# Kernel tuning notes

Hardware: AMD Instinct MI355X
Metric: run time of the kernel (lower is better)

## Reference

```python
import jax, jax.numpy as jnp
import numpy as np

B, H, OUT = 16384, 1024, 128
W_SCALE = 0.03  # ~1/sqrt(H) so attention logits / softmax stay well-conditioned


def setup_inputs() -> dict:
    key = jax.random.key(0)
    ks = jax.random.split(key, 12)
    return {
        "f1": jax.random.normal(ks[0], (B, H), jnp.float32),
        "f2": jax.random.normal(ks[1], (B, H), jnp.float32),
        "f3": jax.random.normal(ks[2], (B, H), jnp.float32),
        "f4": jax.random.normal(ks[3], (B, H), jnp.float32),
        "Wq": jax.random.normal(ks[4], (H, H), jnp.float32) * W_SCALE,
        "bq": jax.random.normal(ks[5], (H,), jnp.float32) * W_SCALE,
        "Wk": jax.random.normal(ks[6], (H, H), jnp.float32) * W_SCALE,
        "bk": jax.random.normal(ks[7], (H,), jnp.float32) * W_SCALE,
        "Wv": jax.random.normal(ks[8], (H, H), jnp.float32) * W_SCALE,
        "bv": jax.random.normal(ks[9], (H,), jnp.float32) * W_SCALE,
        "Wfc": jax.random.normal(ks[10], (H, OUT), jnp.float32) * W_SCALE,
        "bfc": jax.random.normal(ks[11], (OUT,), jnp.float32) * W_SCALE,
    }


def reference(f1, f2, f3, f4, Wq, bq, Wk, bk, Wv, bv, Wfc, bfc):
    # Stack the 4 backbone features: z [B, 4, H]
    z = jnp.stack([f1, f2, f3, f4], axis=1)
    q = z @ Wq + bq            # [B, 4, H]
    k = z @ Wk + bk            # [B, 4, H]
    v = z @ Wv + bv            # [B, 4, H]
    # Tiny 4x4 self-attention over the 4 model-feature tokens
    score = jax.nn.softmax(jnp.einsum('bth,bsh->bts', q, k), axis=-1)  # [B,4,4]
    att = jnp.einsum('bts,bsh->bth', score, v)                          # [B,4,H]
    x = jnp.sum(att, axis=1)                                            # [B,H]
    out = jax.nn.softmax(x @ Wfc + bfc, axis=-1)                        # [B,OUT]
    return (x, out)
```

## Files before the change

### kernel.cpp

```cpp
#include <hip/hip_runtime.h>
#include <hip/hip_bf16.h>
#include <stdint.h>

#define B_SZ 16384
#define H_SZ 1024
#define OUT_SZ 128

typedef __attribute__((ext_vector_type(4))) float f32x4;
typedef __attribute__((ext_vector_type(8))) _Float16 h16x8;
typedef unsigned short u16;
typedef unsigned int u32;

__device__ __forceinline__ u16 f2h(float f) {
  union { _Float16 h; u16 u; } v; v.h = (_Float16)f; return v.u;
}
__device__ __forceinline__ float h2f(u16 u) {
  union { u16 u; _Float16 h; } v; v.u = u; return (float)v.h;
}
__device__ __forceinline__ u32 pk2(float a, float b) {
  return (u32)f2h(a) | ((u32)f2h(b) << 16);
}

__device__ __forceinline__ void gl_lds16(const void* g, void* l) {
  __builtin_amdgcn_global_load_lds(
      (const __attribute__((address_space(1))) u32*)g,
      (__attribute__((address_space(3))) u32*)l, 16, 0, 0);
}

template<int MODE>
__global__ __launch_bounds__(512, 2) void gemm_nt256(
    const u16* __restrict__ Aptr, const u16* __restrict__ Bptr,
    int K,
    float* __restrict__ ep_f, u16* __restrict__ ep_b,
    const float* __restrict__ ep_v,
    const float* zf0, const float* zf1, const float* zf2, const float* zf3)
{
  constexpr int BM = 256, BN = 256, BK = 64;
  __shared__ __align__(16) u16 sA[2][BM * BK];
  __shared__ __align__(16) u16 sB[2][BN * BK];
  const int tid  = threadIdx.x;
  const int wave = tid >> 6;
  const int lane = tid & 63;
  const int qd   = lane >> 4;
  const int c16  = lane & 15;
  const int bm0  = blockIdx.x * BM;
  const int bn0  = blockIdx.y * BN;
  const int wm   = (wave >> 2) * 128;
  const int wn   = (wave & 3) * 64;
  const size_t FBS = (size_t)B_SZ * H_SZ;

  auto stage = [&](int buf, int k0) {
#pragma unroll
    for (int i = 0; i < 4; ++i) {
      int slot = tid + i * 512;
      int r = slot >> 3, c = slot & 7;
      int cc = c ^ (r & 7);
      {
        int gm = bm0 + r;
        const u16* gp;
        if (MODE == 1)
          gp = Aptr + (size_t)(gm & 3) * FBS + (size_t)(gm >> 2) * H_SZ + (k0 + cc * 8);
        else
          gp = Aptr + (size_t)gm * K + (k0 + cc * 8);
        gl_lds16(gp, &sA[buf][(size_t)(slot & ~63) * 8]);
      }
      {
        int gn = bn0 + r;
        const u16* gp = Bptr + (size_t)gn * K + (k0 + cc * 8);
        gl_lds16(gp, &sB[buf][(size_t)(slot & ~63) * 8]);
      }
    }
  };

  f32x4 acc[8][4];
#pragma unroll
  for (int i = 0; i < 8; ++i)
#pragma unroll
    for (int j = 0; j < 4; ++j)
      acc[i][j] = (f32x4){0.f, 0.f, 0.f, 0.f};

  stage(0, 0);
  __syncthreads();
  int cur = 0;
  for (int k0 = 0; k0 < K; k0 += BK) {
    if (k0 + BK < K) stage(cur ^ 1, k0 + BK);
#pragma unroll
    for (int ks = 0; ks < 2; ++ks) {
      h16x8 af[8], bfr[4];
#pragma unroll
      for (int im = 0; im < 8; ++im) {
        int m = wm + im * 16 + c16;
        af[im] = *(const h16x8*)&sA[cur][m * 64 + (((ks * 4 + qd) ^ (m & 7)) * 8)];
      }
#pragma unroll
      for (int in = 0; in < 4; ++in) {
        int n = wn + in * 16 + c16;
        bfr[in] = *(const h16x8*)&sB[cur][n * 64 + (((ks * 4 + qd) ^ (n & 7)) * 8)];
      }
#pragma unroll
      for (int im = 0; im < 8; ++im)
#pragma unroll
        for (int in = 0; in < 4; ++in)
          acc[im][in] = __builtin_amdgcn_mfma_f32_16x16x32_f16(af[im], bfr[in], acc[im][in], 0, 0, 0);
    }
    __syncthreads();
    cur ^= 1;
  }

  if constexpr (MODE == 1) {
    const float* zf[4] = {zf0, zf1, zf2, zf3};
    const int yg = (int)blockIdx.y * 4 + (wave & 3);
#pragma unroll
    for (int im = 0; im < 8; ++im) {
      int mrow = bm0 + wm + im * 16 + qd * 4;
      size_t b = (size_t)(mrow >> 2);
      float p[4][4];
#pragma unroll
      for (int r = 0; r < 4; ++r)
#pragma unroll
        for (int s = 0; s < 4; ++s) p[r][s] = 0.f;
#pragma unroll
      for (int in = 0; in < 4; ++in) {
        int n = bn0 + wn + in * 16 + c16;
        float akv = ep_v[n];
        float rv[4];
#pragma unroll
        for (int r = 0; r < 4; ++r) rv[r] = acc[im][in][r] + akv;
#pragma unroll
        for (int s = 0; s < 4; ++s) {
          float zv = zf[s][b * H_SZ + n];
#pragma unroll
          for (int r = 0; r < 4; ++r) p[r][s] += rv[r] * zv;
        }
      }
#pragma unroll
      for (int r = 0; r < 4; ++r)
#pragma unroll
        for (int s = 0; s < 4; ++s) {
          float v = p[r][s];
          v += __shfl_xor(v, 1);
          v += __shfl_xor(v, 2);
          v += __shfl_xor(v, 4);
          v += __shfl_xor(v, 8);
          if (c16 == 0) ep_f[(b * 16 + (size_t)(r * 4 + s)) * 16 + yg] = v;
        }
    }
  } else {
#pragma unroll
    for (int im = 0; im < 8; ++im)
#pragma unroll
      for (int in = 0; in < 4; ++in) {
        int n = bn0 + wn + in * 16 + c16;
        float bvv = 4.0f * ep_v[n];
#pragma unroll
        for (int r = 0; r < 4; ++r) {
          int m = bm0 + wm + im * 16 + qd * 4 + r;
          float v = acc[im][in][r] + bvv;
          ep_f[(size_t)m * H_SZ + n] = v;
          ep_b[(size_t)m * H_SZ + n] = f2h(v);
        }
      }
  }
}

template<int MODE>
__global__ __launch_bounds__(256, 4) void gemm_nt(
    const u16* __restrict__ Aptr, const u16* __restrict__ Bptr,
    int N, int K,
    float* __restrict__ ep_f, u16* __restrict__ ep_b,
    const float* __restrict__ ep_v)
{
  constexpr int BM = 128, BN = 128, BK = 32;
  __shared__ __align__(16) u16 sA[2][BM * BK];
  __shared__ __align__(16) u16 sB[2][BN * BK];
  const int tid  = threadIdx.x;
  const int wave = tid >> 6;
  const int lane = tid & 63;
  const int qd   = lane >> 4;
  const int c16  = lane & 15;
  const int bm0  = blockIdx.x * BM;
  const int bn0  = blockIdx.y * BN;
  const int wm   = (wave >> 1) * 64;
  const int wn   = (wave & 1) * 64;

  auto stage = [&](int buf, int k0) {
#pragma unroll
    for (int i = 0; i < 2; ++i) {
      int slot = tid + i * 256;
      int r = slot >> 2, pp = slot & 3;
      int cc = pp ^ ((r >> 1) & 3);
      {
        int gm = bm0 + r;
        const u16* gp = Aptr + (size_t)gm * K + (k0 + cc * 8);
        gl_lds16(gp, &sA[buf][(size_t)(slot & ~63) * 8]);
      }
      {
        int gn = bn0 + r;
        const u16* gp = Bptr + (size_t)gn * K + (k0 + cc * 8);
        gl_lds16(gp, &sB[buf][(size_t)(slot & ~63) * 8]);
      }
    }
  };

  f32x4 acc[4][4];
#pragma unroll
  for (int i = 0; i < 4; ++i)
#pragma unroll
    for (int j = 0; j < 4; ++j)
      acc[i][j] = (f32x4){0.f, 0.f, 0.f, 0.f};

  stage(0, 0);
  __syncthreads();
  int cur = 0;
  for (int k0 = 0; k0 < K; k0 += BK) {
    if (k0 + BK < K) stage(cur ^ 1, k0 + BK);
    h16x8 af[4], bfr[4];
#pragma unroll
    for (int im = 0; im < 4; ++im) {
      int m = wm + im * 16 + c16;
      int slot = m * 4 + (qd ^ ((m >> 1) & 3));
      af[im] = *(const h16x8*)&sA[cur][slot * 8];
    }
#pragma unroll
    for (int in = 0; in < 4; ++in) {
      int n = wn + in * 16 + c16;
      int slot = n * 4 + (qd ^ ((n >> 1) & 3));
      bfr[in] = *(const h16x8*)&sB[cur][slot * 8];
    }
#pragma unroll
    for (int im = 0; im < 4; ++im)
#pragma unroll
      for (int in = 0; in < 4; ++in)
        acc[im][in] = __builtin_amdgcn_mfma_f32_16x16x32_f16(af[im], bfr[in], acc[im][in], 0, 0, 0);
    __syncthreads();
    cur ^= 1;
  }

  if constexpr (MODE == 0) {
#pragma unroll
    for (int im = 0; im < 4; ++im)
#pragma unroll
      for (int in = 0; in < 4; ++in) {
        int n = bn0 + wn + in * 16 + c16;
#pragma unroll
        for (int r = 0; r < 4; ++r) {
          int m = bm0 + wm + im * 16 + qd * 4 + r;
          ep_b[(size_t)m * N + n] = f2h(acc[im][in][r]);
        }
      }
  } else {
#pragma unroll
    for (int im = 0; im < 4; ++im)
#pragma unroll
      for (int in = 0; in < 4; ++in) {
        int n = bn0 + wn + in * 16 + c16;
        float bc = ep_v[n];
#pragma unroll
        for (int r = 0; r < 4; ++r) {
          int m = bm0 + wm + im * 16 + qd * 4 + r;
          ep_f[(size_t)m * N + n] = acc[im][in][r] + bc;
        }
      }
  }
}

__global__ __launch_bounds__(256) void prep_weights(
    const float* __restrict__ Wq, const float* __restrict__ Wk,
    const float* __restrict__ Wv, const float* __restrict__ Wfc,
    const float* __restrict__ bq,
    u16* __restrict__ Wq16, u16* __restrict__ Wk16,
    u16* __restrict__ WvT, u16* __restrict__ WfcT,
    float* __restrict__ ak)
{
  __shared__ float t[32][33];
  int blk = blockIdx.x, tid = threadIdx.x;
  if (blk < 2048) {
    const float* src = (blk < 1024) ? Wq : Wk;
    u16* dst = (blk < 1024) ? Wq16 : Wk16;
    size_t i0 = (size_t)(blk & 1023) * 1024 + tid * 4;
    float4 v = *(const float4*)(src + i0);
    *(uint2*)(dst + i0) = make_uint2(pk2(v.x, v.y), pk2(v.z, v.w));
  } else if (blk < 3200) {
    int lx = tid & 31, ly = tid >> 5;
    if (blk < 3072) {
      int ti = blk - 2048;
      int tx = ti & 31, ty = ti >> 5;
#pragma unroll
      for (int k = 0; k < 4; ++k)
        t[ly + 8 * k][lx] = Wv[(size_t)(ty * 32 + ly + 8 * k) * 1024 + tx * 32 + lx];
      __syncthreads();
#pragma unroll
      for (int k = 0; k < 4; ++k)
        WvT[(size_t)(tx * 32 + ly + 8 * k) * 1024 + ty * 32 + lx] = f2h(t[lx][ly + 8 * k]);
    } else {
      int ti = blk - 3072;
      int tx = ti & 3, ty = ti >> 2;
#pragma unroll
      for (int k = 0; k < 4; ++k)
        t[ly + 8 * k][lx] = Wfc[(size_t)(ty * 32 + ly + 8 * k) * 128 + tx * 32 + lx];
      __syncthreads();
#pragma unroll
      for (int k = 0; k < 4; ++k)
        WfcT[(size_t)(tx * 32 + ly + 8 * k) * 1024 + ty * 32 + lx] = f2h(t[lx][ly + 8 * k]);
    }
  } else {
    int wave = tid >> 6, lane = tid & 63;
    int row = (blk - 3200) * 4 + wave;
    float s = 0.f;
    for (int i = lane; i < 1024; i += 64)
      s += Wk[(size_t)row * 1024 + i] * bq[i];
#pragma unroll
    for (int m = 1; m < 64; m <<= 1) s += __shfl_xor(s, m);
    if (lane == 0) ak[row] = s;
  }
}

__global__ __launch_bounds__(256) void convert4(
    const float* __restrict__ f1, const float* __restrict__ f2,
    const float* __restrict__ f3, const float* __restrict__ f4,
    u16* __restrict__ Zh)
{
  int a = blockIdx.x >> 13;
  const float* f = (a == 0) ? f1 : (a == 1) ? f2 : (a == 2) ? f3 : f4;
  size_t off = (size_t)(blockIdx.x & 8191) * 2048 + threadIdx.x * 8;
  float4 v0 = *(const float4*)(f + off);
  float4 v1 = *(const float4*)(f + off + 4);
  *(uint4*)(Zh + (size_t)a * B_SZ * H_SZ + off) =
      make_uint4(pk2(v0.x, v0.y), pk2(v0.z, v0.w), pk2(v1.x, v1.y), pk2(v1.z, v1.w));
}

__global__ __launch_bounds__(256) void softmax_g(
    const float* __restrict__ pl, const u16* __restrict__ Zh,
    u16* __restrict__ G)
{
  const size_t FBS = (size_t)B_SZ * H_SZ;
  int wave = threadIdx.x >> 6, lane = threadIdx.x & 63;
  size_t b = (size_t)blockIdx.x * 4 + wave;
  float4 pv = *(const float4*)(pl + b * 256 + (size_t)lane * 4);
  float part = pv.x + pv.y + pv.z + pv.w;
  part += __shfl_xor(part, 1);
  part += __shfl_xor(part, 2);
  float l[16];
#pragma unroll
  for (int i = 0; i < 16; ++i) l[i] = __shfl(part, i * 4);
  float w0 = 0, w1 = 0, w2 = 0, w3 = 0;
#pragma unroll
  for (int t = 0; t < 4; ++t) {
    float a0 = l[t * 4], a1 = l[t * 4 + 1], a2 = l[t * 4 + 2], a3 = l[t * 4 + 3];
    float mx = fmaxf(fmaxf(a0, a1), fmaxf(a2, a3));
    float e0 = __expf(a0 - mx), e1 = __expf(a1 - mx), e2 = __expf(a2 - mx), e3 = __expf(a3 - mx);
    float inv = 1.0f / (e0 + e1 + e2 + e3);
    w0 += e0 * inv; w1 += e1 * inv; w2 += e2 * inv; w3 += e3 * inv;
  }
#pragma unroll
  for (int ch = 0; ch < 2; ++ch) {
    size_t h0 = (size_t)lane * 8 + ch * 512;
    float g[8];
#pragma unroll
    for (int j = 0; j < 8; ++j) g[j] = 0.f;
#pragma unroll
    for (int s = 0; s < 4; ++s) {
      float ws = (s == 0) ? w0 : (s == 1) ? w1 : (s == 2) ? w2 : w3;
      uint4 zz = *(const uint4*)(Zh + (size_t)s * FBS + b * H_SZ + h0);
      u32 zs[4] = {zz.x, zz.y, zz.z, zz.w};
#pragma unroll
      for (int j = 0; j < 4; ++j) {
        g[2 * j]     += ws * h2f((u16)(zs[j] & 0xffffu));
        g[2 * j + 1] += ws * h2f((u16)(zs[j] >> 16));
      }
    }
    *(uint4*)(G + b * H_SZ + h0) =
        make_uint4(pk2(g[0], g[1]), pk2(g[2], g[3]), pk2(g[4], g[5]), pk2(g[6], g[7]));
  }
}

__global__ __launch_bounds__(256) void softmax_out(
    const float* __restrict__ L2, float* __restrict__ out)
{
  int wave = threadIdx.x >> 6, lane = threadIdx.x & 63;
  size_t row = (size_t)blockIdx.x * 4 + wave;
  float2 v = *(const float2*)(L2 + row * 128 + lane * 2);
  float mx = fmaxf(v.x, v.y);
#pragma unroll
  for (int m = 1; m < 64; m <<= 1) mx = fmaxf(mx, __shfl_xor(mx, m));
  float e0 = __expf(v.x - mx), e1 = __expf(v.y - mx);
  float s = e0 + e1;
#pragma unroll
  for (int m = 1; m < 64; m <<= 1) s += __shfl_xor(s, m);
  float inv = 1.0f / s;
  *(float2*)(out + row * 128 + lane * 2) = make_float2(e0 * inv, e1 * inv);
}

extern "C" void kernel_launch(void* const* d_in, const int* in_sizes, int n_in,
                              void* d_out, int out_size, void* d_ws, size_t ws_size,
                              hipStream_t stream)
{
  const float* f1  = (const float*)d_in[0];
  const float* f2  = (const float*)d_in[1];
  const float* f3  = (const float*)d_in[2];
  const float* f4  = (const float*)d_in[3];
  const float* Wq  = (const float*)d_in[4];
  const float* bq  = (const float*)d_in[5];
  const float* Wk  = (const float*)d_in[6];
  const float* Wv  = (const float*)d_in[8];
  const float* bv  = (const float*)d_in[9];
  const float* Wfc = (const float*)d_in[10];
  const float* bfc = (const float*)d_in[11];

  float* x_out = (float*)d_out;
  float* out2  = x_out + (size_t)B_SZ * H_SZ;

  const size_t BH = (size_t)B_SZ * H_SZ;
  const size_t HH = (size_t)H_SZ * H_SZ;
  char* w = (char*)d_ws;
  u16* Zh   = (u16*)w;  w += 4 * BH * sizeof(u16);
  u16* G    = (u16*)w;  w += BH * sizeof(u16);
  u16* Xh   = (u16*)w;  w += BH * sizeof(u16);
  u16* Wq16 = (u16*)w;  w += HH * 2;
  u16* Wk16 = (u16*)w;  w += HH * 2;
  u16* AT   = (u16*)w;  w += HH * 2;
  u16* WvT  = (u16*)w;  w += HH * 2;
  u16* WfcT = (u16*)w;  w += (size_t)OUT_SZ * H_SZ * 2;
  float* ak  = (float*)w;  w += H_SZ * sizeof(float);
  float* fcl = (float*)w;  w += (size_t)B_SZ * OUT_SZ * sizeof(float);
  float* pl  = (float*)Xh;

  prep_weights<<<3456, 256, 0, stream>>>(Wq, Wk, Wv, Wfc, bq,
      Wq16, Wk16, WvT, WfcT, ak);
  convert4<<<32768, 256, 0, stream>>>(f1, f2, f3, f4, Zh);
  gemm_nt<0><<<dim3(8, 8), 256, 0, stream>>>(
      Wk16, Wq16, 1024, 1024, nullptr, AT, nullptr);
  gemm_nt256<1><<<dim3(256, 4), 512, 0, stream>>>(
      Zh, AT, 1024, pl, nullptr, ak, f1, f2, f3, f4);
  softmax_g<<<4096, 256, 0, stream>>>(pl, Zh, G);
  gemm_nt256<2><<<dim3(64, 4), 512, 0, stream>>>(
      G, WvT, 1024, x_out, Xh, bv,
      nullptr, nullptr, nullptr, nullptr);
  gemm_nt<3><<<dim3(128, 1), 256, 0, stream>>>(
      Xh, WfcT, 128, 1024, fcl, nullptr, bfc);
  softmax_out<<<4096, 256, 0, stream>>>(fcl, out2);
}
```

Before: 686.0 us.

## Deepen GEMM pipeline to 4-stage LDS ring with vmcnt waits and fp16 epilogue reads

Reworks the main 256x256 GEMM loop so that BK drops to 32 and LDS uses a 4-buffer ring prefetched three tiles ahead. The full-block __syncthreads plus double buffer is replaced by s_waitcnt vmcnt with a single barrier per tile, and s_setprio is raised around the MFMA block. The swizzle is adapted to the narrower tile, and K is now a compile-time constant. The MODE 1 epilogue reads the fp16 Z copy instead of the fp32 features, which halves that traffic but adds fp16 rounding to the attention-score dot products.

```diff
diff --git a/kernel.cpp b/kernel.cpp
--- a/kernel.cpp
+++ b/kernel.cpp
@@ -30,14 +30,12 @@
 template<int MODE>
 __global__ __launch_bounds__(512, 2) void gemm_nt256(
     const u16* __restrict__ Aptr, const u16* __restrict__ Bptr,
-    int K,
     float* __restrict__ ep_f, u16* __restrict__ ep_b,
-    const float* __restrict__ ep_v,
-    const float* zf0, const float* zf1, const float* zf2, const float* zf3)
-{
-  constexpr int BM = 256, BN = 256, BK = 64;
-  __shared__ __align__(16) u16 sA[2][BM * BK];
-  __shared__ __align__(16) u16 sB[2][BN * BK];
+    const float* __restrict__ ep_v, const u16* __restrict__ Zep)
+{
+  constexpr int BM = 256, BN = 256, BK = 32, K = 1024, NT = K / BK;
+  __shared__ __align__(16) u16 sA[4][BM * BK];
+  __shared__ __align__(16) u16 sB[4][BN * BK];
   const int tid  = threadIdx.x;
   const int wave = tid >> 6;
   const int lane = tid & 63;
@@ -49,12 +47,13 @@
   const int wn   = (wave & 3) * 64;
   const size_t FBS = (size_t)B_SZ * H_SZ;
 
-  auto stage = [&](int buf, int k0) {
-#pragma unroll
-    for (int i = 0; i < 4; ++i) {
+  auto stage = [&](int buf, int t) {
+    const int k0 = t * BK;
+#pragma unroll
+    for (int i = 0; i < 2; ++i) {
       int slot = tid + i * 512;
-      int r = slot >> 3, c = slot & 7;
-      int cc = c ^ (r & 7);
+      int r = slot >> 2, c = slot & 3;
+      int cc = c ^ ((r >> 1) & 3);
       {
         int gm = bm0 + r;
         const u16* gp;
@@ -80,35 +79,41 @@
       acc[i][j] = (f32x4){0.f, 0.f, 0.f, 0.f};
 
   stage(0, 0);
-  __syncthreads();
-  int cur = 0;
-  for (int k0 = 0; k0 < K; k0 += BK) {
-    if (k0 + BK < K) stage(cur ^ 1, k0 + BK);
-#pragma unroll
-    for (int ks = 0; ks < 2; ++ks) {
-      h16x8 af[8], bfr[4];
-#pragma unroll
-      for (int im = 0; im < 8; ++im) {
-        int m = wm + im * 16 + c16;
-        af[im] = *(const h16x8*)&sA[cur][m * 64 + (((ks * 4 + qd) ^ (m & 7)) * 8)];
-      }
-#pragma unroll
-      for (int in = 0; in < 4; ++in) {
-        int n = wn + in * 16 + c16;
-        bfr[in] = *(const h16x8*)&sB[cur][n * 64 + (((ks * 4 + qd) ^ (n & 7)) * 8)];
-      }
-#pragma unroll
-      for (int im = 0; im < 8; ++im)
-#pragma unroll
-        for (int in = 0; in < 4; ++in)
-          acc[im][in] = __builtin_amdgcn_mfma_f32_16x16x32_f16(af[im], bfr[in], acc[im][in], 0, 0, 0);
-    }
-    __syncthreads();
-    cur ^= 1;
+  stage(1, 1);
+  stage(2, 2);
+
+  for (int t = 0; t < NT; ++t) {
+    const int buf = t & 3;
+    if (t + 2 < NT)      asm volatile("s_waitcnt vmcnt(8)" ::: "memory");
+    else if (t + 1 < NT) asm volatile("s_waitcnt vmcnt(4)" ::: "memory");
+    else                 asm volatile("s_waitcnt vmcnt(0)" ::: "memory");
+    __builtin_amdgcn_s_barrier();
+    asm volatile("" ::: "memory");
+    if (t + 3 < NT) stage((t + 3) & 3, t + 3);
+
+    h16x8 af[8], bfr[4];
+#pragma unroll
+    for (int im = 0; im < 8; ++im) {
+      int m = wm + im * 16 + c16;
+      int slot = m * 4 + (qd ^ ((m >> 1) & 3));
+      af[im] = *(const h16x8*)&sA[buf][slot * 8];
+    }
+#pragma unroll
+    for (int in = 0; in < 4; ++in) {
+      int n = wn + in * 16 + c16;
+      int slot = n * 4 + (qd ^ ((n >> 1) & 3));
+      bfr[in] = *(const h16x8*)&sB[buf][slot * 8];
+    }
+    __builtin_amdgcn_s_setprio(1);
+#pragma unroll
+    for (int im = 0; im < 8; ++im)
+#pragma unroll
+      for (int in = 0; in < 4; ++in)
+        acc[im][in] = __builtin_amdgcn_mfma_f32_16x16x32_f16(af[im], bfr[in], acc[im][in], 0, 0, 0);
+    __builtin_amdgcn_s_setprio(0);
   }
 
   if constexpr (MODE == 1) {
-    const float* zf[4] = {zf0, zf1, zf2, zf3};
     const int yg = (int)blockIdx.y * 4 + (wave & 3);
 #pragma unroll
     for (int im = 0; im < 8; ++im) {
@@ -128,7 +133,7 @@
         for (int r = 0; r < 4; ++r) rv[r] = acc[im][in][r] + akv;
 #pragma unroll
         for (int s = 0; s < 4; ++s) {
-          float zv = zf[s][b * H_SZ + n];
+          float zv = h2f(Zep[(size_t)s * FBS + b * H_SZ + n]);
 #pragma unroll
           for (int r = 0; r < 4; ++r) p[r][s] += rv[r] * zv;
         }
@@ -431,11 +436,10 @@
   gemm_nt<0><<<dim3(8, 8), 256, 0, stream>>>(
       Wk16, Wq16, 1024, 1024, nullptr, AT, nullptr);
   gemm_nt256<1><<<dim3(256, 4), 512, 0, stream>>>(
-      Zh, AT, 1024, pl, nullptr, ak, f1, f2, f3, f4);
+      Zh, AT, pl, nullptr, ak, Zh);
   softmax_g<<<4096, 256, 0, stream>>>(pl, Zh, G);
   gemm_nt256<2><<<dim3(64, 4), 512, 0, stream>>>(
-      G, WvT, 1024, x_out, Xh, bv,
-      nullptr, nullptr, nullptr, nullptr);
+      G, WvT, x_out, Xh, bv, nullptr);
   gemm_nt<3><<<dim3(128, 1), 256, 0, stream>>>(
       Xh, WfcT, 128, 1024, fcl, nullptr, bfc);
   softmax_out<<<4096, 256, 0, stream>>>(fcl, out2);
```

Result: no change. 678.9 us (-1.0%).

## Retile big GEMMs to 64x512 blocks and read fp16 Z in epilogue

Applied to the files above, without the earlier changes.

Replaces the 256x256x64 GEMM tile with a 64x512x32 tile in which all eight waves share the same 64 rows. The grid grows and launch bounds allow four blocks per SM, which lowers register pressure and raises occupancy. The MODE 1 epilogue now reads the fp16 converted Z buffer instead of the four fp32 feature arrays, halving those reads at some loss of precision. Smaller M tiles mean less reuse of the B operand, so each block reloads more weight data.

```diff
diff --git a/kernel.cpp b/kernel.cpp
--- a/kernel.cpp
+++ b/kernel.cpp
@@ -28,14 +28,12 @@
 }
 
 template<int MODE>
-__global__ __launch_bounds__(512, 2) void gemm_nt256(
+__global__ __launch_bounds__(512, 4) void gemm_nt64(
     const u16* __restrict__ Aptr, const u16* __restrict__ Bptr,
-    int K,
     float* __restrict__ ep_f, u16* __restrict__ ep_b,
-    const float* __restrict__ ep_v,
-    const float* zf0, const float* zf1, const float* zf2, const float* zf3)
-{
-  constexpr int BM = 256, BN = 256, BK = 64;
+    const float* __restrict__ ep_v, const u16* __restrict__ Zep)
+{
+  constexpr int BM = 64, BN = 512, BK = 32, K = 1024;
   __shared__ __align__(16) u16 sA[2][BM * BK];
   __shared__ __align__(16) u16 sB[2][BN * BK];
   const int tid  = threadIdx.x;
@@ -45,36 +43,36 @@
   const int c16  = lane & 15;
   const int bm0  = blockIdx.x * BM;
   const int bn0  = blockIdx.y * BN;
-  const int wm   = (wave >> 2) * 128;
-  const int wn   = (wave & 3) * 64;
+  const int wn   = wave * 64;
   const size_t FBS = (size_t)B_SZ * H_SZ;
 
   auto stage = [&](int buf, int k0) {
+    if (tid < 256) {
+      int slot = tid;
+      int r = slot >> 2, c = slot & 3;
+      int cc = c ^ ((r >> 1) & 3);
+      int gm = bm0 + r;
+      const u16* gp;
+      if (MODE == 1)
+        gp = Aptr + (size_t)(gm & 3) * FBS + (size_t)(gm >> 2) * H_SZ + (k0 + cc * 8);
+      else
+        gp = Aptr + (size_t)gm * K + (k0 + cc * 8);
+      gl_lds16(gp, &sA[buf][(size_t)(slot & ~63) * 8]);
+    }
 #pragma unroll
     for (int i = 0; i < 4; ++i) {
       int slot = tid + i * 512;
-      int r = slot >> 3, c = slot & 7;
-      int cc = c ^ (r & 7);
-      {
-        int gm = bm0 + r;
-        const u16* gp;
-        if (MODE == 1)
-          gp = Aptr + (size_t)(gm & 3) * FBS + (size_t)(gm >> 2) * H_SZ + (k0 + cc * 8);
-        else
-          gp = Aptr + (size_t)gm * K + (k0 + cc * 8);
-        gl_lds16(gp, &sA[buf][(size_t)(slot & ~63) * 8]);
-      }
-      {
-        int gn = bn0 + r;
-        const u16* gp = Bptr + (size_t)gn * K + (k0 + cc * 8);
-        gl_lds16(gp, &sB[buf][(size_t)(slot & ~63) * 8]);
-      }
+      int r = slot >> 2, c = slot & 3;
+      int cc = c ^ ((r >> 1) & 3);
+      int gn = bn0 + r;
+      const u16* gp = Bptr + (size_t)gn * K + (k0 + cc * 8);
+      gl_lds16(gp, &sB[buf][(size_t)(slot & ~63) * 8]);
     }
   };
 
-  f32x4 acc[8][4];
-#pragma unroll
-  for (int i = 0; i < 8; ++i)
+  f32x4 acc[4][4];
+#pragma unroll
+  for (int i = 0; i < 4; ++i)
 #pragma unroll
     for (int j = 0; j < 4; ++j)
       acc[i][j] = (f32x4){0.f, 0.f, 0.f, 0.f};
@@ -84,35 +82,33 @@
   int cur = 0;
   for (int k0 = 0; k0 < K; k0 += BK) {
     if (k0 + BK < K) stage(cur ^ 1, k0 + BK);
-#pragma unroll
-    for (int ks = 0; ks < 2; ++ks) {
-      h16x8 af[8], bfr[4];
-#pragma unroll
-      for (int im = 0; im < 8; ++im) {
-        int m = wm + im * 16 + c16;
-        af[im] = *(const h16x8*)&sA[cur][m * 64 + (((ks * 4 + qd) ^ (m & 7)) * 8)];
-      }
-#pragma unroll
-      for (int in = 0; in < 4; ++in) {
-        int n = wn + in * 16 + c16;
-        bfr[in] = *(const h16x8*)&sB[cur][n * 64 + (((ks * 4 + qd) ^ (n & 7)) * 8)];
-      }
-#pragma unroll
-      for (int im = 0; im < 8; ++im)
-#pragma unroll
-        for (int in = 0; in < 4; ++in)
-          acc[im][in] = __builtin_amdgcn_mfma_f32_16x16x32_f16(af[im], bfr[in], acc[im][in], 0, 0, 0);
-    }
+    h16x8 af[4], bfr[4];
+#pragma unroll
+    for (int im = 0; im < 4; ++im) {
+      int m = im * 16 + c16;
+      int slot = m * 4 + (qd ^ ((m >> 1) & 3));
+      af[im] = *(const h16x8*)&sA[cur][slot * 8];
+    }
+#pragma unroll
+    for (int in = 0; in < 4; ++in) {
+      int n = wn + in * 16 + c16;
+      int slot = n * 4 + (qd ^ ((n >> 1) & 3));
+      bfr[in] = *(const h16x8*)&sB[cur][slot * 8];
+    }
+#pragma unroll
+    for (int im = 0; im < 4; ++im)
+#pragma unroll
+      for (int in = 0; in < 4; ++in)
+        acc[im][in] = __builtin_amdgcn_mfma_f32_16x16x32_f16(af[im], bfr[in], acc[im][in], 0, 0, 0);
     __syncthreads();
     cur ^= 1;
   }
 
   if constexpr (MODE == 1) {
-    const float* zf[4] = {zf0, zf1, zf2, zf3};
-    const int yg = (int)blockIdx.y * 4 + (wave & 3);
-#pragma unroll
-    for (int im = 0; im < 8; ++im) {
-      int mrow = bm0 + wm + im * 16 + qd * 4;
+    const int yg = (int)blockIdx.y * 8 + wave;
+#pragma unroll
+    for (int im = 0; im < 4; ++im) {
+      int mrow = bm0 + im * 16 + qd * 4;
       size_t b = (size_t)(mrow >> 2);
       float p[4][4];
 #pragma unroll
@@ -128,7 +124,7 @@
         for (int r = 0; r < 4; ++r) rv[r] = acc[im][in][r] + akv;
 #pragma unroll
         for (int s = 0; s < 4; ++s) {
-          float zv = zf[s][b * H_SZ + n];
+          float zv = h2f(Zep[(size_t)s * FBS + b * H_SZ + n]);
 #pragma unroll
           for (int r = 0; r < 4; ++r) p[r][s] += rv[r] * zv;
         }
@@ -147,14 +143,14 @@
     }
   } else {
 #pragma unroll
-    for (int im = 0; im < 8; ++im)
+    for (int im = 0; im < 4; ++im)
 #pragma unroll
       for (int in = 0; in < 4; ++in) {
         int n = bn0 + wn + in * 16 + c16;
         float bvv = 4.0f * ep_v[n];
 #pragma unroll
         for (int r = 0; r < 4; ++r) {
-          int m = bm0 + wm + im * 16 + qd * 4 + r;
+          int m = bm0 + im * 16 + qd * 4 + r;
           float v = acc[im][in][r] + bvv;
           ep_f[(size_t)m * H_SZ + n] = v;
           ep_b[(size_t)m * H_SZ + n] = f2h(v);
@@ -430,12 +426,11 @@
   convert4<<<32768, 256, 0, stream>>>(f1, f2, f3, f4, Zh);
   gemm_nt<0><<<dim3(8, 8), 256, 0, stream>>>(
       Wk16, Wq16, 1024, 1024, nullptr, AT, nullptr);
-  gemm_nt256<1><<<dim3(256, 4), 512, 0, stream>>>(
-      Zh, AT, 1024, pl, nullptr, ak, f1, f2, f3, f4);
+  gemm_nt64<1><<<dim3(1024, 2), 512, 0, stream>>>(
+      Zh, AT, pl, nullptr, ak, Zh);
   softmax_g<<<4096, 256, 0, stream>>>(pl, Zh, G);
-  gemm_nt256<2><<<dim3(64, 4), 512, 0, stream>>>(
-      G, WvT, 1024, x_out, Xh, bv,
-      nullptr, nullptr, nullptr, nullptr);
+  gemm_nt64<2><<<dim3(256, 2), 512, 0, stream>>>(
+      G, WvT, x_out, Xh, bv, nullptr);
   gemm_nt<3><<<dim3(128, 1), 256, 0, stream>>>(
       Xh, WfcT, 128, 1024, fcl, nullptr, bfc);
   softmax_out<<<4096, 256, 0, stream>>>(fcl, out2);
```

New measurement: 690.6 us. About the same (+0.7%).
